# Optimization experiments

Measured on AMD Instinct MI355X. Metric: run time of the kernel, lower is better.

Reference implementation:

```python
import jax, jax.numpy as jnp
import numpy as np

H = 51  # hidden size hard-coded in the original module


def _lstm_cell(x, h, c, Wi, Wh, bi, bh):
    # torch LSTMCell: gates = x@Wi^T + bi + h@Wh^T + bh, chunks [i, f, g, o]
    g = x @ Wi.T + bi + h @ Wh.T + bh
    i, f, gg, o = jnp.split(g, 4, axis=1)
    c_new = jax.nn.sigmoid(f) * c + jax.nn.sigmoid(i) * jnp.tanh(gg)
    h_new = jax.nn.sigmoid(o) * jnp.tanh(c_new)
    return h_new, c_new


def setup_inputs() -> dict:
    key = jax.random.key(0)
    ks = jax.random.split(key, 12)
    B, T = 512, 1024
    s = 0.1
    return {
        "input": jax.random.normal(ks[0], (B, T), dtype=jnp.float32),
        "W_ih1": jax.random.normal(ks[1], (4 * H, 1), dtype=jnp.float32) * s,
        "W_hh1": jax.random.normal(ks[2], (4 * H, H), dtype=jnp.float32) * s,
        "b_ih1": jax.random.normal(ks[3], (4 * H,), dtype=jnp.float32) * s,
        "b_hh1": jax.random.normal(ks[4], (4 * H,), dtype=jnp.float32) * s,
        "W_ih2": jax.random.normal(ks[5], (4 * H, H), dtype=jnp.float32) * s,
        "W_hh2": jax.random.normal(ks[6], (4 * H, H), dtype=jnp.float32) * s,
        "b_ih2": jax.random.normal(ks[7], (4 * H,), dtype=jnp.float32) * s,
        "b_hh2": jax.random.normal(ks[8], (4 * H,), dtype=jnp.float32) * s,
        "W_lin": jax.random.normal(ks[9], (1, H), dtype=jnp.float32) * s,
        "b_lin": jax.random.normal(ks[10], (1,), dtype=jnp.float32) * s,
        "future": 64,
    }


def reference(input, W_ih1, W_hh1, b_ih1, b_hh1, W_ih2, W_hh2, b_ih2, b_hh2,
              W_lin, b_lin, future):
    B = input.shape[0]
    h1 = jnp.zeros((B, H), dtype=input.dtype)
    c1 = jnp.zeros((B, H), dtype=input.dtype)
    h2 = jnp.zeros((B, H), dtype=input.dtype)
    c2 = jnp.zeros((B, H), dtype=input.dtype)

    def step(carry, x_t):
        h1, c1, h2, c2 = carry
        h1, c1 = _lstm_cell(x_t, h1, c1, W_ih1, W_hh1, b_ih1, b_hh1)
        h2, c2 = _lstm_cell(h1, h2, c2, W_ih2, W_hh2, b_ih2, b_hh2)
        out = h2 @ W_lin.T + b_lin  # [B, 1]
        return (h1, c1, h2, c2), out

    xs = input.T[:, :, None]  # [T, B, 1] timestep-major
    carry, outs = jax.lax.scan(step, (h1, c1, h2, c2), xs)
    last_out = outs[-1]  # [B, 1]

    def fstep(carry, _):
        h1, c1, h2, c2, out = carry
        h1, c1 = _lstm_cell(out, h1, c1, W_ih1, W_hh1, b_ih1, b_hh1)
        h2, c2 = _lstm_cell(h1, h2, c2, W_ih2, W_hh2, b_ih2, b_hh2)
        out = h2 @ W_lin.T + b_lin
        return (h1, c1, h2, c2, out), out

    _, fouts = jax.lax.scan(fstep, (*carry, last_out), None, length=future)
    all_outs = jnp.concatenate([outs, fouts], axis=0)  # [T+future, B, 1]
    return all_outs[:, :, 0].T  # [B, T+future]
```

## Files before the change

### kernel.cpp

```cpp
#include <hip/hip_runtime.h>
#include <math.h>

#define HID 51
#define TMAIN 1024
#define FUT 64
#define TT (TMAIN + FUT)
#define RING 128
#define RPAD 68

typedef float v2f __attribute__((ext_vector_type(2)));

__device__ __forceinline__ float fast_sigmoid(float x) {
  return 1.0f / (1.0f + __expf(-x));
}
__device__ __forceinline__ float fast_tanh(float x) {
  return 1.0f - 2.0f / (__expf(2.0f * x) + 1.0f);
}

__device__ __forceinline__ void dot2x(const float* hA, const float* hB,
                                      const v2f (&w2)[2][25],
                                      const float (&w50)[2],
                                      float (&aA)[2], float (&aB)[2]) {
  const float4* a4 = reinterpret_cast<const float4*>(hA);
  const float4* b4 = reinterpret_cast<const float4*>(hB);
  v2f sA0 = {0.f, 0.f}, sA1 = {0.f, 0.f};
  v2f sB0 = {0.f, 0.f}, sB1 = {0.f, 0.f};
#pragma unroll
  for (int q = 0; q < 12; ++q) {
    float4 av = a4[q];
    float4 bv = b4[q];
    v2f alo = {av.x, av.y}, ahi = {av.z, av.w};
    v2f blo = {bv.x, bv.y}, bhi = {bv.z, bv.w};
    sA0 = __builtin_elementwise_fma(alo, w2[0][2 * q + 0], sA0);
    sB0 = __builtin_elementwise_fma(blo, w2[0][2 * q + 0], sB0);
    sA1 = __builtin_elementwise_fma(alo, w2[1][2 * q + 0], sA1);
    sB1 = __builtin_elementwise_fma(blo, w2[1][2 * q + 0], sB1);
    sA0 = __builtin_elementwise_fma(ahi, w2[0][2 * q + 1], sA0);
    sB0 = __builtin_elementwise_fma(bhi, w2[0][2 * q + 1], sB0);
    sA1 = __builtin_elementwise_fma(ahi, w2[1][2 * q + 1], sA1);
    sB1 = __builtin_elementwise_fma(bhi, w2[1][2 * q + 1], sB1);
  }
  float4 at = a4[12];
  float4 bt = b4[12];
  v2f alo = {at.x, at.y}, blo = {bt.x, bt.y};
  sA0 = __builtin_elementwise_fma(alo, w2[0][24], sA0);
  sB0 = __builtin_elementwise_fma(blo, w2[0][24], sB0);
  sA1 = __builtin_elementwise_fma(alo, w2[1][24], sA1);
  sB1 = __builtin_elementwise_fma(blo, w2[1][24], sB1);
  aA[0] = fmaf(at.z, w50[0], aA[0] + sA0.x + sA0.y);
  aB[0] = fmaf(bt.z, w50[0], aB[0] + sB0.x + sB0.y);
  aA[1] = fmaf(at.z, w50[1], aA[1] + sA1.x + sA1.y);
  aB[1] = fmaf(bt.z, w50[1], aB[1] + sB1.x + sB1.y);
}

__device__ __forceinline__ void dotH(const float* hA, const float* hB,
                                     const v2f (&w)[2][13],
                                     float (&aA)[2], float (&aB)[2]) {
  const float2* a2 = reinterpret_cast<const float2*>(hA);
  const float2* b2 = reinterpret_cast<const float2*>(hB);
  v2f sA0 = {0.f, 0.f}, sA1 = {0.f, 0.f};
  v2f sB0 = {0.f, 0.f}, sB1 = {0.f, 0.f};
#pragma unroll
  for (int p = 0; p < 13; ++p) {
    float2 av = a2[p], bv = b2[p];
    v2f a = {av.x, av.y}, b = {bv.x, bv.y};
    sA0 = __builtin_elementwise_fma(a, w[0][p], sA0);
    sB0 = __builtin_elementwise_fma(b, w[0][p], sB0);
    sA1 = __builtin_elementwise_fma(a, w[1][p], sA1);
    sB1 = __builtin_elementwise_fma(b, w[1][p], sB1);
  }
  aA[0] = sA0.x + sA0.y;
  aB[0] = sB0.x + sB0.y;
  aA[1] = sA1.x + sA1.y;
  aB[1] = sB1.x + sB1.y;
}

__global__ __launch_bounds__(512, 2)
void lstm2_persistent(const float* __restrict__ input,
                      const float* __restrict__ Wi1,
                      const float* __restrict__ Wh1,
                      const float* __restrict__ bi1,
                      const float* __restrict__ bh1,
                      const float* __restrict__ Wi2,
                      const float* __restrict__ Wh2,
                      const float* __restrict__ bi2,
                      const float* __restrict__ bh2,
                      const float* __restrict__ Wlin,
                      const float* __restrict__ blin,
                      float* __restrict__ out) {
  __shared__ __align__(16) float lds_x[2][TMAIN];
  __shared__ __align__(16) float lds_h1[2][2][64];
  __shared__ __align__(16) float lds_piS[2][2][64][12];
  __shared__ __align__(16) float lds_h2h[RING][2][RPAD];
  __shared__ __align__(16) float lds_wlin[64];
  __shared__ __align__(16) float lds_outbuf[2][64];
  __shared__ float lds_lin[2][2][2];
  __shared__ float lds_fb[2];

  const int tid = threadIdx.x;
  const int s0 = blockIdx.x * 2;
  const int wid = tid >> 6;
  const int lane = tid & 63;
  const int half = lane >> 5;
  const int l5 = lane & 31;
  const int base = (wid & 1) * 26;
  const int nu = (wid & 1) ? 25 : 26;
  const bool act = l5 < nu;
  const int u = base + (act ? l5 : 0);
  const int g0 = half * 2;
  const int koff = (wid >= 6) ? 0 : 26;
  const int kh = (wid >= 6) ? 0 : 1;

  for (int i = tid; i < TMAIN; i += 512) {
    lds_x[0][i] = input[s0 * TMAIN + i];
    lds_x[1][i] = input[(s0 + 1) * TMAIN + i];
  }
  if (tid < 64) {
    lds_h1[0][0][tid] = 0.0f;
    lds_h1[0][1][tid] = 0.0f;
    lds_h1[1][0][tid] = 0.0f;
    lds_h1[1][1][tid] = 0.0f;
    lds_wlin[tid] = (tid < HID) ? Wlin[tid] : 0.0f;
  }
  if (tid < 128) lds_h2h[RING - 1][tid >> 6][tid & 63] = 0.0f;

  v2f w2f[2][25];
  float w50f[2] = {0.f, 0.f};
  v2f w2h[2][13];
  float bias[2] = {0.f, 0.f};
  float wi1g[2] = {0.f, 0.f};
  float wlin_u = 0.0f;
  float cA = 0.0f, cB = 0.0f;

  if (wid < 4) {
    const float* Wsel = (wid < 2) ? Wh1 : Wh2;
#pragma unroll
    for (int g = 0; g < 2; ++g) {
      const float* row = Wsel + ((g0 + g) * HID + u) * HID;
#pragma unroll
      for (int p = 0; p < 25; ++p) {
        v2f t;
        t.x = row[2 * p + 0];
        t.y = row[2 * p + 1];
        w2f[g][p] = t;
      }
      w50f[g] = row[50];
    }
    if (wid < 2) {
#pragma unroll
      for (int g = 0; g < 2; ++g) {
        bias[g] = bi1[(g0 + g) * HID + u] + bh1[(g0 + g) * HID + u];
        wi1g[g] = Wi1[(g0 + g) * HID + u];
      }
    } else {
      wlin_u = Wlin[u];
    }
#pragma unroll
    for (int g = 0; g < 2; ++g) {
#pragma unroll
      for (int p = 0; p < 25; ++p) asm volatile("" : "+v"(w2f[g][p]));
      asm volatile("" : "+v"(w50f[g]), "+v"(bias[g]), "+v"(wi1g[g]));
    }
    asm volatile("" : "+v"(wlin_u));
  } else {
#pragma unroll
    for (int g = 0; g < 2; ++g) {
      const float* row = Wi2 + ((g0 + g) * HID + u) * HID + koff;
      if (koff == 0) {
#pragma unroll
        for (int p = 0; p < 13; ++p) {
          v2f t;
          t.x = row[2 * p + 0];
          t.y = row[2 * p + 1];
          w2h[g][p] = t;
        }
      } else {
#pragma unroll
        for (int p = 0; p < 12; ++p) {
          v2f t;
          t.x = row[2 * p + 0];
          t.y = row[2 * p + 1];
          w2h[g][p] = t;
        }
        v2f t;
        t.x = row[24];
        t.y = 0.0f;
        w2h[g][12] = t;
      }
    }
    if (kh == 1) {
#pragma unroll
      for (int g = 0; g < 2; ++g)
        bias[g] = bi2[(g0 + g) * HID + u] + bh2[(g0 + g) * HID + u];
    }
#pragma unroll
    for (int g = 0; g < 2; ++g) {
#pragma unroll
      for (int p = 0; p < 13; ++p) asm volatile("" : "+v"(w2h[g][p]));
      asm volatile("" : "+v"(bias[g]));
    }
  }
  const float blin_s = blin[0];

  __syncthreads();

  for (int k = 0; k <= TMAIN + 2; ++k) {
    if (wid < 2) {
      if (k < TMAIN) {
        float xA = lds_x[0][k], xB = lds_x[1][k];
        float aA[2], aB[2];
#pragma unroll
        for (int g = 0; g < 2; ++g) {
          aA[g] = fmaf(xA, wi1g[g], bias[g]);
          aB[g] = fmaf(xB, wi1g[g], bias[g]);
        }
        dot2x(lds_h1[k & 1][0], lds_h1[k & 1][1], w2f, w50f, aA, aB);
        float pA0 = __shfl_xor(aA[0], 32), pA1 = __shfl_xor(aA[1], 32);
        float pB0 = __shfl_xor(aB[0], 32), pB1 = __shfl_xor(aB[1], 32);
        float giA = half ? pA0 : aA[0], gfA = half ? pA1 : aA[1];
        float ggA = half ? aA[0] : pA0, goA = half ? aA[1] : pA1;
        float giB = half ? pB0 : aB[0], gfB = half ? pB1 : aB[1];
        float ggB = half ? aB[0] : pB0, goB = half ? aB[1] : pB1;
        cA = fast_sigmoid(gfA) * cA + fast_sigmoid(giA) * fast_tanh(ggA);
        cB = fast_sigmoid(gfB) * cB + fast_sigmoid(giB) * fast_tanh(ggB);
        float hA = fast_sigmoid(goA) * fast_tanh(cA);
        float hB = fast_sigmoid(goB) * fast_tanh(cB);
        if (act && half == 0) {
          lds_h1[(k + 1) & 1][0][u] = hA;
          lds_h1[(k + 1) & 1][1][u] = hB;
        }
      }
    } else if (wid < 4) {
      if (k >= 2 && k <= TMAIN + 1) {
        const int m2 = k - 2;
        const int pm = m2 & 1;
        float4 vA = *reinterpret_cast<const float4*>(&lds_piS[pm][0][u][2 * g0]);
        float4 vB = *reinterpret_cast<const float4*>(&lds_piS[pm][1][u][2 * g0]);
        float aA[2], aB[2];
        aA[0] = vA.x + vA.y;
        aA[1] = vA.z + vA.w;
        aB[0] = vB.x + vB.y;
        aB[1] = vB.z + vB.w;
        dot2x(&lds_h2h[(m2 - 1) & (RING - 1)][0][0],
              &lds_h2h[(m2 - 1) & (RING - 1)][1][0], w2f, w50f, aA, aB);
        float pA0 = __shfl_xor(aA[0], 32), pA1 = __shfl_xor(aA[1], 32);
        float pB0 = __shfl_xor(aB[0], 32), pB1 = __shfl_xor(aB[1], 32);
        float giA = half ? pA0 : aA[0], gfA = half ? pA1 : aA[1];
        float ggA = half ? aA[0] : pA0, goA = half ? aA[1] : pA1;
        float giB = half ? pB0 : aB[0], gfB = half ? pB1 : aB[1];
        float ggB = half ? aB[0] : pB0, goB = half ? aB[1] : pB1;
        cA = fast_sigmoid(gfA) * cA + fast_sigmoid(giA) * fast_tanh(ggA);
        cB = fast_sigmoid(gfB) * cB + fast_sigmoid(giB) * fast_tanh(ggB);
        float hA = fast_sigmoid(goA) * fast_tanh(cA);
        float hB = fast_sigmoid(goB) * fast_tanh(cB);
        if (act && half == 0) {
          lds_h2h[m2 & (RING - 1)][0][u] = hA;
          lds_h2h[m2 & (RING - 1)][1][u] = hB;
        }
      }
    } else {
      if (k >= 1 && k <= TMAIN) {
        float aA[2], aB[2];
        dotH(&lds_h1[k & 1][0][koff], &lds_h1[k & 1][1][koff], w2h, aA, aB);
        const int pm = (k - 1) & 1;
        if (act) {
          if (kh == 1) {
            aA[0] += bias[0];
            aA[1] += bias[1];
            aB[0] += bias[0];
            aB[1] += bias[1];
          }
          lds_piS[pm][0][u][2 * (g0 + 0) + kh] = aA[0];
          lds_piS[pm][0][u][2 * (g0 + 1) + kh] = aA[1];
          lds_piS[pm][1][u][2 * (g0 + 0) + kh] = aB[0];
          lds_piS[pm][1][u][2 * (g0 + 1) + kh] = aB[1];
        }
      }
      if (wid < 6 && k >= 66 && ((k - 66) & 63) == 0) {
        const int c = k - 66;
        const int seq = wid - 4;
        const int m = c + lane;
        const float* r = &lds_h2h[m & (RING - 1)][seq][0];
        float o0 = 0.f, o1 = 0.f;
#pragma unroll
        for (int j = 0; j < 48; j += 2) {
          o0 = fmaf(lds_wlin[j], r[j], o0);
          o1 = fmaf(lds_wlin[j + 1], r[j + 1], o1);
        }
        o0 = fmaf(lds_wlin[48], r[48], o0);
        o1 = fmaf(lds_wlin[49], r[49], o1);
        o0 = fmaf(lds_wlin[50], r[50], o0);
        float o = o0 + o1 + blin_s;
        out[(s0 + seq) * TT + m] = o;
        if (m == TMAIN - 1) lds_fb[seq] = o;
      }
    }
    __syncthreads();
  }

  for (int t = TMAIN; t < TT; ++t) {
    float phA[2] = {0.f, 0.f}, phB[2] = {0.f, 0.f};
    if (wid < 2) {
      float oA, oB;
      if (t == TMAIN) {
        oA = lds_fb[0];
        oB = lds_fb[1];
      } else {
        oA = lds_lin[(t - 1) & 1][0][0] + lds_lin[(t - 1) & 1][0][1] + blin_s;
        oB = lds_lin[(t - 1) & 1][1][0] + lds_lin[(t - 1) & 1][1][1] + blin_s;
        if (lane == 0) {
          if (wid == 0) lds_outbuf[0][t - 1 - TMAIN] = oA;
          else          lds_outbuf[1][t - 1 - TMAIN] = oB;
        }
      }
      float aA[2], aB[2];
#pragma unroll
      for (int g = 0; g < 2; ++g) {
        aA[g] = fmaf(oA, wi1g[g], bias[g]);
        aB[g] = fmaf(oB, wi1g[g], bias[g]);
      }
      dot2x(lds_h1[t & 1][0], lds_h1[t & 1][1], w2f, w50f, aA, aB);
      float pA0 = __shfl_xor(aA[0], 32), pA1 = __shfl_xor(aA[1], 32);
      float pB0 = __shfl_xor(aB[0], 32), pB1 = __shfl_xor(aB[1], 32);
      float giA = half ? pA0 : aA[0], gfA = half ? pA1 : aA[1];
      float ggA = half ? aA[0] : pA0, goA = half ? aA[1] : pA1;
      float giB = half ? pB0 : aB[0], gfB = half ? pB1 : aB[1];
      float ggB = half ? aB[0] : pB0, goB = half ? aB[1] : pB1;
      cA = fast_sigmoid(gfA) * cA + fast_sigmoid(giA) * fast_tanh(ggA);
      cB = fast_sigmoid(gfB) * cB + fast_sigmoid(giB) * fast_tanh(ggB);
      float hA = fast_sigmoid(goA) * fast_tanh(cA);
      float hB = fast_sigmoid(goB) * fast_tanh(cB);
      if (act && half == 0) {
        lds_h1[(t + 1) & 1][0][u] = hA;
        lds_h1[(t + 1) & 1][1][u] = hB;
      }
    } else if (wid < 4) {
      dot2x(&lds_h2h[(t - 1) & (RING - 1)][0][0],
            &lds_h2h[(t - 1) & (RING - 1)][1][0], w2f, w50f, phA, phB);
    }
    __syncthreads();
    if (wid >= 4) {
      float aA[2], aB[2];
      dotH(&lds_h1[(t + 1) & 1][0][koff], &lds_h1[(t + 1) & 1][1][koff], w2h,
           aA, aB);
      const int pm = t & 1;
      if (act) {
        if (kh == 1) {
          aA[0] += bias[0];
          aA[1] += bias[1];
          aB[0] += bias[0];
          aB[1] += bias[1];
        }
        lds_piS[pm][0][u][2 * (g0 + 0) + kh] = aA[0];
        lds_piS[pm][0][u][2 * (g0 + 1) + kh] = aA[1];
        lds_piS[pm][1][u][2 * (g0 + 0) + kh] = aB[0];
        lds_piS[pm][1][u][2 * (g0 + 1) + kh] = aB[1];
      }
    }
    __syncthreads();
    if (wid >= 2 && wid < 4) {
      const int pm = t & 1;
      float4 vA = *reinterpret_cast<const float4*>(&lds_piS[pm][0][u][2 * g0]);
      float4 vB = *reinterpret_cast<const float4*>(&lds_piS[pm][1][u][2 * g0]);
      float aA[2], aB[2];
      aA[0] = vA.x + vA.y + phA[0];
      aA[1] = vA.z + vA.w + phA[1];
      aB[0] = vB.x + vB.y + phB[0];
      aB[1] = vB.z + vB.w + phB[1];
      float pA0 = __shfl_xor(aA[0], 32), pA1 = __shfl_xor(aA[1], 32);
      float pB0 = __shfl_xor(aB[0], 32), pB1 = __shfl_xor(aB[1], 32);
      float giA = half ? pA0 : aA[0], gfA = half ? pA1 : aA[1];
      float ggA = half ? aA[0] : pA0, goA = half ? aA[1] : pA1;
      float giB = half ? pB0 : aB[0], gfB = half ? pB1 : aB[1];
      float ggB = half ? aB[0] : pB0, goB = half ? aB[1] : pB1;
      cA = fast_sigmoid(gfA) * cA + fast_sigmoid(giA) * fast_tanh(ggA);
      cB = fast_sigmoid(gfB) * cB + fast_sigmoid(giB) * fast_tanh(ggB);
      float hA = fast_sigmoid(goA) * fast_tanh(cA);
      float hB = fast_sigmoid(goB) * fast_tanh(cB);
      float val = 0.0f;
      if (act) {
        if (half == 0) {
          lds_h2h[t & (RING - 1)][0][u] = hA;
          val = wlin_u * hA;
        } else {
          lds_h2h[t & (RING - 1)][1][u] = hB;
          val = wlin_u * hB;
        }
      }
#pragma unroll
      for (int off = 16; off >= 1; off >>= 1) val += __shfl_xor(val, off);
      if (lane == 0) lds_lin[t & 1][0][wid - 2] = val;
      if (lane == 32) lds_lin[t & 1][1][wid - 2] = val;
    }
    __syncthreads();
  }

  if (wid < 2 && lane == 0) {
    float o = lds_lin[(TT - 1) & 1][wid][0] + lds_lin[(TT - 1) & 1][wid][1] +
              blin_s;
    lds_outbuf[wid][63] = o;
  }
  __syncthreads();
  if (wid == 4 || wid == 5) {
    const int seq = wid - 4;
    out[(s0 + seq) * TT + TMAIN + lane] = lds_outbuf[seq][lane];
  }
}

extern "C" void kernel_launch(void* const* d_in, const int* in_sizes, int n_in,
                              void* d_out, int out_size, void* d_ws,
                              size_t ws_size, hipStream_t stream) {
  const float* input = (const float*)d_in[0];
  const float* Wi1 = (const float*)d_in[1];
  const float* Wh1 = (const float*)d_in[2];
  const float* bi1 = (const float*)d_in[3];
  const float* bh1 = (const float*)d_in[4];
  const float* Wi2 = (const float*)d_in[5];
  const float* Wh2 = (const float*)d_in[6];
  const float* bi2 = (const float*)d_in[7];
  const float* bh2 = (const float*)d_in[8];
  const float* Wlin = (const float*)d_in[9];
  const float* blin = (const float*)d_in[10];
  float* out = (float*)d_out;

  const int B = in_sizes[0] / TMAIN;
  lstm2_persistent<<<B / 2, 512, 0, stream>>>(input, Wi1, Wh1, bi1, bh1, Wi2,
                                              Wh2, bi2, bh2, Wlin, blin, out);
}
```

Measured before the change: 1.392 ms.

## Replace per-step block barriers with LDS flag-based producer-consumer sync in main loop

In the 1024-step main loop, each wave group (layer-1 recurrence, layer-2 input projection, layer-2 recurrence) now runs its own loop and synchronises through per-wave LDS progress counters polled with s_sleep, instead of a __syncthreads every step. The h1 and pre-activation buffers grow from double to four-deep rings so producers can run a few steps ahead. The pre-activation buffer is split into two transposed arrays, one per K-half, and the output linear dot is vectorised with float4. The aim is to remove the full-block barrier latency from the serial critical path and let pipeline stages drift. The risk is spin-wait overhead and memory-ordering subtleties around the volatile LDS flags.

```diff
diff --git a/kernel.cpp b/kernel.cpp
--- a/kernel.cpp
+++ b/kernel.cpp
@@ -15,6 +15,26 @@
 }
 __device__ __forceinline__ float fast_tanh(float x) {
   return 1.0f - 2.0f / (__expf(2.0f * x) + 1.0f);
+}
+
+__device__ __forceinline__ void flag_publish(volatile int* f, bool lane0,
+                                             int v) {
+  asm volatile("s_waitcnt lgkmcnt(0)" ::: "memory");
+  if (lane0) *f = v;
+}
+__device__ __forceinline__ void wait1(volatile int* f, int tgt) {
+  while (*f < tgt) __builtin_amdgcn_s_sleep(1);
+  asm volatile("" ::: "memory");
+}
+__device__ __forceinline__ void wait2(volatile int* a, volatile int* b,
+                                      int tgt) {
+  while (*a < tgt || *b < tgt) __builtin_amdgcn_s_sleep(1);
+  asm volatile("" ::: "memory");
+}
+__device__ __forceinline__ void wait4(volatile int* f, int tgt) {
+  while (f[0] < tgt || f[1] < tgt || f[2] < tgt || f[3] < tgt)
+    __builtin_amdgcn_s_sleep(1);
+  asm volatile("" ::: "memory");
 }
 
 __device__ __forceinline__ void dot2x(const float* hA, const float* hB,
@@ -89,13 +109,17 @@
                       const float* __restrict__ blin,
                       float* __restrict__ out) {
   __shared__ __align__(16) float lds_x[2][TMAIN];
-  __shared__ __align__(16) float lds_h1[2][2][64];
-  __shared__ __align__(16) float lds_piS[2][2][64][12];
+  __shared__ __align__(16) float lds_h1[4][2][64];
+  __shared__ __align__(16) float lds_piK1[4][2][4][64];
+  __shared__ __align__(16) float lds_piK2[4][2][4][64];
   __shared__ __align__(16) float lds_h2h[RING][2][RPAD];
   __shared__ __align__(16) float lds_wlin[64];
   __shared__ __align__(16) float lds_outbuf[2][64];
   __shared__ float lds_lin[2][2][2];
   __shared__ float lds_fb[2];
+  __shared__ int lds_flags[8];
+
+  volatile int* vf = (volatile int*)lds_flags;
 
   const int tid = threadIdx.x;
   const int s0 = blockIdx.x * 2;
@@ -116,13 +140,15 @@
     lds_x[1][i] = input[(s0 + 1) * TMAIN + i];
   }
   if (tid < 64) {
-    lds_h1[0][0][tid] = 0.0f;
-    lds_h1[0][1][tid] = 0.0f;
-    lds_h1[1][0][tid] = 0.0f;
-    lds_h1[1][1][tid] = 0.0f;
+#pragma unroll
+    for (int p = 0; p < 4; ++p) {
+      lds_h1[p][0][tid] = 0.0f;
+      lds_h1[p][1][tid] = 0.0f;
+    }
     lds_wlin[tid] = (tid < HID) ? Wlin[tid] : 0.0f;
   }
   if (tid < 128) lds_h2h[RING - 1][tid >> 6][tid & 63] = 0.0f;
+  if (tid < 8) lds_flags[tid] = -1;
 
   v2f w2f[2][25];
   float w50f[2] = {0.f, 0.f};
@@ -204,99 +230,119 @@
 
   __syncthreads();
 
-  for (int k = 0; k <= TMAIN + 2; ++k) {
-    if (wid < 2) {
-      if (k < TMAIN) {
-        float xA = lds_x[0][k], xB = lds_x[1][k];
-        float aA[2], aB[2];
-#pragma unroll
-        for (int g = 0; g < 2; ++g) {
-          aA[g] = fmaf(xA, wi1g[g], bias[g]);
-          aB[g] = fmaf(xB, wi1g[g], bias[g]);
-        }
-        dot2x(lds_h1[k & 1][0], lds_h1[k & 1][1], w2f, w50f, aA, aB);
-        float pA0 = __shfl_xor(aA[0], 32), pA1 = __shfl_xor(aA[1], 32);
-        float pB0 = __shfl_xor(aB[0], 32), pB1 = __shfl_xor(aB[1], 32);
-        float giA = half ? pA0 : aA[0], gfA = half ? pA1 : aA[1];
-        float ggA = half ? aA[0] : pA0, goA = half ? aA[1] : pA1;
-        float giB = half ? pB0 : aB[0], gfB = half ? pB1 : aB[1];
-        float ggB = half ? aB[0] : pB0, goB = half ? aB[1] : pB1;
-        cA = fast_sigmoid(gfA) * cA + fast_sigmoid(giA) * fast_tanh(ggA);
-        cB = fast_sigmoid(gfB) * cB + fast_sigmoid(giB) * fast_tanh(ggB);
-        float hA = fast_sigmoid(goA) * fast_tanh(cA);
-        float hB = fast_sigmoid(goB) * fast_tanh(cB);
-        if (act && half == 0) {
-          lds_h1[(k + 1) & 1][0][u] = hA;
-          lds_h1[(k + 1) & 1][1][u] = hB;
-        }
-      }
-    } else if (wid < 4) {
-      if (k >= 2 && k <= TMAIN + 1) {
-        const int m2 = k - 2;
-        const int pm = m2 & 1;
-        float4 vA = *reinterpret_cast<const float4*>(&lds_piS[pm][0][u][2 * g0]);
-        float4 vB = *reinterpret_cast<const float4*>(&lds_piS[pm][1][u][2 * g0]);
-        float aA[2], aB[2];
-        aA[0] = vA.x + vA.y;
-        aA[1] = vA.z + vA.w;
-        aB[0] = vB.x + vB.y;
-        aB[1] = vB.z + vB.w;
-        dot2x(&lds_h2h[(m2 - 1) & (RING - 1)][0][0],
-              &lds_h2h[(m2 - 1) & (RING - 1)][1][0], w2f, w50f, aA, aB);
-        float pA0 = __shfl_xor(aA[0], 32), pA1 = __shfl_xor(aA[1], 32);
-        float pB0 = __shfl_xor(aB[0], 32), pB1 = __shfl_xor(aB[1], 32);
-        float giA = half ? pA0 : aA[0], gfA = half ? pA1 : aA[1];
-        float ggA = half ? aA[0] : pA0, goA = half ? aA[1] : pA1;
-        float giB = half ? pB0 : aB[0], gfB = half ? pB1 : aB[1];
-        float ggB = half ? aB[0] : pB0, goB = half ? aB[1] : pB1;
-        cA = fast_sigmoid(gfA) * cA + fast_sigmoid(giA) * fast_tanh(ggA);
-        cB = fast_sigmoid(gfB) * cB + fast_sigmoid(giB) * fast_tanh(ggB);
-        float hA = fast_sigmoid(goA) * fast_tanh(cA);
-        float hB = fast_sigmoid(goB) * fast_tanh(cB);
-        if (act && half == 0) {
-          lds_h2h[m2 & (RING - 1)][0][u] = hA;
-          lds_h2h[m2 & (RING - 1)][1][u] = hB;
-        }
-      }
-    } else {
-      if (k >= 1 && k <= TMAIN) {
-        float aA[2], aB[2];
-        dotH(&lds_h1[k & 1][0][koff], &lds_h1[k & 1][1][koff], w2h, aA, aB);
-        const int pm = (k - 1) & 1;
-        if (act) {
-          if (kh == 1) {
-            aA[0] += bias[0];
-            aA[1] += bias[1];
-            aB[0] += bias[0];
-            aB[1] += bias[1];
-          }
-          lds_piS[pm][0][u][2 * (g0 + 0) + kh] = aA[0];
-          lds_piS[pm][0][u][2 * (g0 + 1) + kh] = aA[1];
-          lds_piS[pm][1][u][2 * (g0 + 0) + kh] = aB[0];
-          lds_piS[pm][1][u][2 * (g0 + 1) + kh] = aB[1];
-        }
-      }
-      if (wid < 6 && k >= 66 && ((k - 66) & 63) == 0) {
-        const int c = k - 66;
-        const int seq = wid - 4;
+  if (wid < 2) {
+    volatile int* fOther = vf + (1 - wid);
+    for (int k = 0; k < TMAIN; ++k) {
+      wait1(fOther, k - 1);
+      wait4(vf + 4, k - 4);
+      float xA = lds_x[0][k], xB = lds_x[1][k];
+      float aA[2], aB[2];
+#pragma unroll
+      for (int g = 0; g < 2; ++g) {
+        aA[g] = fmaf(xA, wi1g[g], bias[g]);
+        aB[g] = fmaf(xB, wi1g[g], bias[g]);
+      }
+      dot2x(lds_h1[k & 3][0], lds_h1[k & 3][1], w2f, w50f, aA, aB);
+      float pA0 = __shfl_xor(aA[0], 32), pA1 = __shfl_xor(aA[1], 32);
+      float pB0 = __shfl_xor(aB[0], 32), pB1 = __shfl_xor(aB[1], 32);
+      float giA = half ? pA0 : aA[0], gfA = half ? pA1 : aA[1];
+      float ggA = half ? aA[0] : pA0, goA = half ? aA[1] : pA1;
+      float giB = half ? pB0 : aB[0], gfB = half ? pB1 : aB[1];
+      float ggB = half ? aB[0] : pB0, goB = half ? aB[1] : pB1;
+      cA = fast_sigmoid(gfA) * cA + fast_sigmoid(giA) * fast_tanh(ggA);
+      cB = fast_sigmoid(gfB) * cB + fast_sigmoid(giB) * fast_tanh(ggB);
+      float hA = fast_sigmoid(goA) * fast_tanh(cA);
+      float hB = fast_sigmoid(goB) * fast_tanh(cB);
+      if (act && half == 0) {
+        lds_h1[(k + 1) & 3][0][u] = hA;
+        lds_h1[(k + 1) & 3][1][u] = hB;
+      }
+      flag_publish(vf + wid, lane == 0, k);
+    }
+  } else if (wid >= 4) {
+    const int seq = wid - 4;
+    for (int j = 0; j < TMAIN; ++j) {
+      wait2(vf + 0, vf + 1, j);
+      wait2(vf + 2, vf + 3, j - 4);
+      float aA[2], aB[2];
+      dotH(&lds_h1[(j + 1) & 3][0][koff], &lds_h1[(j + 1) & 3][1][koff], w2h,
+           aA, aB);
+      const int pm = j & 3;
+      if (act) {
+        if (kh == 1) {
+          aA[0] += bias[0];
+          aA[1] += bias[1];
+          aB[0] += bias[0];
+          aB[1] += bias[1];
+          lds_piK2[pm][0][g0 + 0][u] = aA[0];
+          lds_piK2[pm][0][g0 + 1][u] = aA[1];
+          lds_piK2[pm][1][g0 + 0][u] = aB[0];
+          lds_piK2[pm][1][g0 + 1][u] = aB[1];
+        } else {
+          lds_piK1[pm][0][g0 + 0][u] = aA[0];
+          lds_piK1[pm][0][g0 + 1][u] = aA[1];
+          lds_piK1[pm][1][g0 + 0][u] = aB[0];
+          lds_piK1[pm][1][g0 + 1][u] = aB[1];
+        }
+      }
+      flag_publish(vf + wid, lane == 0, j);
+      if (wid < 6 && (j & 63) == 63) {
+        const int c = j - 63;
+        wait2(vf + 2, vf + 3, j);
         const int m = c + lane;
         const float* r = &lds_h2h[m & (RING - 1)][seq][0];
-        float o0 = 0.f, o1 = 0.f;
-#pragma unroll
-        for (int j = 0; j < 48; j += 2) {
-          o0 = fmaf(lds_wlin[j], r[j], o0);
-          o1 = fmaf(lds_wlin[j + 1], r[j + 1], o1);
-        }
-        o0 = fmaf(lds_wlin[48], r[48], o0);
-        o1 = fmaf(lds_wlin[49], r[49], o1);
-        o0 = fmaf(lds_wlin[50], r[50], o0);
-        float o = o0 + o1 + blin_s;
+        const float4* r4 = reinterpret_cast<const float4*>(r);
+        const float4* w4 = reinterpret_cast<const float4*>(lds_wlin);
+        float o0 = 0.f, o1 = 0.f, o2 = 0.f, o3 = 0.f;
+#pragma unroll
+        for (int q = 0; q < 12; ++q) {
+          float4 rv = r4[q];
+          float4 wv = w4[q];
+          o0 = fmaf(rv.x, wv.x, o0);
+          o1 = fmaf(rv.y, wv.y, o1);
+          o2 = fmaf(rv.z, wv.z, o2);
+          o3 = fmaf(rv.w, wv.w, o3);
+        }
+        o0 = fmaf(r[48], lds_wlin[48], o0);
+        o1 = fmaf(r[49], lds_wlin[49], o1);
+        o2 = fmaf(r[50], lds_wlin[50], o2);
+        float o = (o0 + o1) + (o2 + o3) + blin_s;
         out[(s0 + seq) * TT + m] = o;
         if (m == TMAIN - 1) lds_fb[seq] = o;
       }
     }
-    __syncthreads();
-  }
+  } else {
+    volatile int* fOther = vf + (5 - wid);
+    for (int m = 0; m < TMAIN; ++m) {
+      wait4(vf + 4, m);
+      wait1(fOther, m - 1);
+      const int pm = m & 3;
+      float aA[2], aB[2];
+      aA[0] = lds_piK1[pm][0][g0 + 0][u] + lds_piK2[pm][0][g0 + 0][u];
+      aA[1] = lds_piK1[pm][0][g0 + 1][u] + lds_piK2[pm][0][g0 + 1][u];
+      aB[0] = lds_piK1[pm][1][g0 + 0][u] + lds_piK2[pm][1][g0 + 0][u];
+      aB[1] = lds_piK1[pm][1][g0 + 1][u] + lds_piK2[pm][1][g0 + 1][u];
+      dot2x(&lds_h2h[(m - 1) & (RING - 1)][0][0],
+            &lds_h2h[(m - 1) & (RING - 1)][1][0], w2f, w50f, aA, aB);
+      float pA0 = __shfl_xor(aA[0], 32), pA1 = __shfl_xor(aA[1], 32);
+      float pB0 = __shfl_xor(aB[0], 32), pB1 = __shfl_xor(aB[1], 32);
+      float giA = half ? pA0 : aA[0], gfA = half ? pA1 : aA[1];
+      float ggA = half ? aA[0] : pA0, goA = half ? aA[1] : pA1;
+      float giB = half ? pB0 : aB[0], gfB = half ? pB1 : aB[1];
+      float ggB = half ? aB[0] : pB0, goB = half ? aB[1] : pB1;
+      cA = fast_sigmoid(gfA) * cA + fast_sigmoid(giA) * fast_tanh(ggA);
+      cB = fast_sigmoid(gfB) * cB + fast_sigmoid(giB) * fast_tanh(ggB);
+      float hA = fast_sigmoid(goA) * fast_tanh(cA);
+      float hB = fast_sigmoid(goB) * fast_tanh(cB);
+      if (act && half == 0) {
+        lds_h2h[m & (RING - 1)][0][u] = hA;
+        lds_h2h[m & (RING - 1)][1][u] = hB;
+      }
+      flag_publish(vf + wid, lane == 0, m);
+    }
+  }
+
+  __syncthreads();
 
   for (int t = TMAIN; t < TT; ++t) {
     float phA[2] = {0.f, 0.f}, phB[2] = {0.f, 0.f};
@@ -319,7 +365,7 @@
         aA[g] = fmaf(oA, wi1g[g], bias[g]);
         aB[g] = fmaf(oB, wi1g[g], bias[g]);
       }
-      dot2x(lds_h1[t & 1][0], lds_h1[t & 1][1], w2f, w50f, aA, aB);
+      dot2x(lds_h1[t & 3][0], lds_h1[t & 3][1], w2f, w50f, aA, aB);
       float pA0 = __shfl_xor(aA[0], 32), pA1 = __shfl_xor(aA[1], 32);
       float pB0 = __shfl_xor(aB[0], 32), pB1 = __shfl_xor(aB[1], 32);
       float giA = half ? pA0 : aA[0], gfA = half ? pA1 : aA[1];
@@ -331,8 +377,8 @@
       float hA = fast_sigmoid(goA) * fast_tanh(cA);
       float hB = fast_sigmoid(goB) * fast_tanh(cB);
       if (act && half == 0) {
-        lds_h1[(t + 1) & 1][0][u] = hA;
-        lds_h1[(t + 1) & 1][1][u] = hB;
+        lds_h1[(t + 1) & 3][0][u] = hA;
+        lds_h1[(t + 1) & 3][1][u] = hB;
       }
     } else if (wid < 4) {
       dot2x(&lds_h2h[(t - 1) & (RING - 1)][0][0],
@@ -341,32 +387,35 @@
     __syncthreads();
     if (wid >= 4) {
       float aA[2], aB[2];
-      dotH(&lds_h1[(t + 1) & 1][0][koff], &lds_h1[(t + 1) & 1][1][koff], w2h,
+      dotH(&lds_h1[(t + 1) & 3][0][koff], &lds_h1[(t + 1) & 3][1][koff], w2h,
            aA, aB);
-      const int pm = t & 1;
+      const int pm = t & 3;
       if (act) {
         if (kh == 1) {
           aA[0] += bias[0];
           aA[1] += bias[1];
           aB[0] += bias[0];
           aB[1] += bias[1];
-        }
-        lds_piS[pm][0][u][2 * (g0 + 0) + kh] = aA[0];
-        lds_piS[pm][0][u][2 * (g0 + 1) + kh] = aA[1];
-        lds_piS[pm][1][u][2 * (g0 + 0) + kh] = aB[0];
-        lds_piS[pm][1][u][2 * (g0 + 1) + kh] = aB[1];
+          lds_piK2[pm][0][g0 + 0][u] = aA[0];
+          lds_piK2[pm][0][g0 + 1][u] = aA[1];
+          lds_piK2[pm][1][g0 + 0][u] = aB[0];
+          lds_piK2[pm][1][g0 + 1][u] = aB[1];
+        } else {
+          lds_piK1[pm][0][g0 + 0][u] = aA[0];
+          lds_piK1[pm][0][g0 + 1][u] = aA[1];
+          lds_piK1[pm][1][g0 + 0][u] = aB[0];
+          lds_piK1[pm][1][g0 + 1][u] = aB[1];
+        }
       }
     }
     __syncthreads();
     if (wid >= 2 && wid < 4) {
-      const int pm = t & 1;
-      float4 vA = *reinterpret_cast<const float4*>(&lds_piS[pm][0][u][2 * g0]);
-      float4 vB = *reinterpret_cast<const float4*>(&lds_piS[pm][1][u][2 * g0]);
-      float aA[2], aB[2];
-      aA[0] = vA.x + vA.y + phA[0];
-      aA[1] = vA.z + vA.w + phA[1];
-      aB[0] = vB.x + vB.y + phB[0];
-      aB[1] = vB.z + vB.w + phB[1];
+      const int pm = t & 3;
+      float aA[2], aB[2];
+      aA[0] = lds_piK1[pm][0][g0 + 0][u] + lds_piK2[pm][0][g0 + 0][u] + phA[0];
+      aA[1] = lds_piK1[pm][0][g0 + 1][u] + lds_piK2[pm][0][g0 + 1][u] + phA[1];
+      aB[0] = lds_piK1[pm][1][g0 + 0][u] + lds_piK2[pm][1][g0 + 0][u] + phB[0];
+      aB[1] = lds_piK1[pm][1][g0 + 1][u] + lds_piK2[pm][1][g0 + 1][u] + phB[1];
       float pA0 = __shfl_xor(aA[0], 32), pA1 = __shfl_xor(aA[1], 32);
       float pB0 = __shfl_xor(aB[0], 32), pB1 = __shfl_xor(aB[1], 32);
       float giA = half ? pA0 : aA[0], gfA = half ? pA1 : aA[1];
```

After: 1.661 ms. +19.3%, slower.
